# Kernel tuning notes

Measured on AMD Instinct MI355X. Metric: run time of the kernel, lower is better.

The kernel has to match this reference:

```python
import jax, jax.numpy as jnp
import numpy as np

N = 10000       # nodes
E = 640000      # edges
D_IN = 128
D_OUT = 128
EPS = 1e-5      # LayerNorm eps (torch default)


def setup_inputs() -> dict:
    key = jax.random.key(0)
    k_x, k_e, k_w, k_b, k_g = jax.random.split(key, 5)
    x = jax.random.normal(k_x, (N, D_IN), dtype=jnp.float32)
    edge_index = jax.random.randint(k_e, (2, E), 0, N, dtype=jnp.int64)
    # GCNConv linear weight (PyG uses glorot) and bias
    lim = float(np.sqrt(6.0 / (D_IN + D_OUT)))
    W = jax.random.uniform(k_w, (D_IN, D_OUT), minval=-lim, maxval=lim, dtype=jnp.float32)
    b = jnp.zeros((D_OUT,), dtype=jnp.float32)
    # LayerNorm affine params
    gamma = jnp.ones((D_OUT,), dtype=jnp.float32)
    beta = jnp.zeros((D_OUT,), dtype=jnp.float32)
    return {"x": x, "edge_index": edge_index, "W": W, "b": b, "gamma": gamma, "beta": beta}


def reference(x, edge_index, W, b, gamma, beta):
    # --- GCNConv: A_hat = D^{-1/2} (A + I) D^{-1/2}; out = A_hat X W + b ---
    self_idx = jnp.arange(N, dtype=edge_index.dtype)
    src = jnp.concatenate([edge_index[0], self_idx])  # [E+N]
    dst = jnp.concatenate([edge_index[1], self_idx])  # [E+N]
    deg = jax.ops.segment_sum(jnp.ones_like(src, dtype=x.dtype), dst, num_segments=N)
    dinv = jnp.where(deg > 0, jax.lax.rsqrt(deg), 0.0)  # [N]
    norm = dinv[src] * dinv[dst]                        # [E+N]
    h = x @ W                                           # [N, D_OUT] transform first (cheaper)
    msg = h[src] * norm[:, None]                        # [E+N, D_OUT]
    out = jax.ops.segment_sum(msg, dst, num_segments=N) + b
    # --- LayerNorm over feature dim ---
    mu = jnp.mean(out, axis=-1, keepdims=True)
    var = jnp.mean(jnp.square(out - mu), axis=-1, keepdims=True)
    out = (out - mu) * jax.lax.rsqrt(var + EPS) * gamma + beta
    # act = Identity (last_act=ReLU is truthy -> Identity branch); dropout = eval identity; residual=False
    return out
```

## Files before the change

kernel.cpp:

```cpp
#include <hip/hip_runtime.h>
#include <hip/hip_fp16.h>

#define D 128
#define LN_EPS 1e-5f


static __device__ __forceinline__ float h2f(unsigned short h) {
    return __half2float(__builtin_bit_cast(__half, h));
}
static __device__ __forceinline__ unsigned short f2h(float f) {
    return __builtin_bit_cast(unsigned short, __float2half_rn(f));
}

static __device__ __forceinline__ void flagbar(int* slots, int c, int C, int phase) {
    __syncthreads();
    int val = 0x5A5A0001 + phase;
    int tid = threadIdx.x;
    if (tid == 0)
        __hip_atomic_store(&slots[phase * 64 + c], val, __ATOMIC_RELEASE, __HIP_MEMORY_SCOPE_AGENT);
    if (tid < C) {
        while (__hip_atomic_load(&slots[phase * 64 + tid], __ATOMIC_ACQUIRE, __HIP_MEMORY_SCOPE_AGENT) != val)
            __builtin_amdgcn_s_sleep(1);
    }
    __syncthreads();
}

#define P1DONE 0x5A5A00B1
#define GMAXR 8

__global__ __launch_bounds__(1024) void build_gemm_kernel(
        const int* __restrict__ src, const int* __restrict__ dst,
        const float* __restrict__ x, const float* __restrict__ W,
        unsigned int* __restrict__ Hh,
        unsigned short* __restrict__ ghist, int* __restrict__ blocksum,
        int* __restrict__ rowptr, float* __restrict__ dinv,
        unsigned short* __restrict__ csr, int* __restrict__ bar,
        int* __restrict__ p1flag,
        int N, int E, int Ec, int C, int G) {
    extern __shared__ int lds[];
    __shared__ int s_scan[20];
    int c = blockIdx.x;
    int tid = threadIdx.x;
    int lane = tid & 63, wv = tid >> 6;

    if (c >= C) {
        unsigned int* sWh = (unsigned int*)lds;
        #pragma unroll
        for (int i = tid; i < D * D / 2; i += 1024) {
            float2 v = ((const float2*)W)[i];
            sWh[i] = (unsigned int)f2h(v.x) | ((unsigned int)f2h(v.y) << 16);
        }
        __syncthreads();
        int gb = c - C;
        int nb = G - C;
        int nper = (N + nb - 1) / nb;
        int r0 = gb * nper;
        int rn = min(nper, N - r0); if (rn < 0) rn = 0;

        float2 acc[GMAXR];
        #pragma unroll
        for (int j = 0; j < GMAXR; j++) {
            acc[j] = make_float2(0.f, 0.f);
            int lr = wv + 16 * j;
            if (lr < rn) {
                float2 xr = ((const float2*)x)[(size_t)(r0 + lr) * 64 + lane];
                float y0 = 0.f, y1 = 0.f;
                #pragma unroll 8
                for (int k = 0; k < 64; k++) {
                    float g0 = __shfl(xr.x, k);
                    float g1 = __shfl(xr.y, k);
                    unsigned int w0 = sWh[(2 * k) * 64 + lane];
                    unsigned int w1 = sWh[(2 * k + 1) * 64 + lane];
                    y0 += g0 * h2f((unsigned short)w0) + g1 * h2f((unsigned short)w1);
                    y1 += g0 * h2f((unsigned short)(w0 >> 16)) + g1 * h2f((unsigned short)(w1 >> 16));
                }
                acc[j] = make_float2(y0, y1);
            }
        }
        if (tid == 0) {
            while (__hip_atomic_load(p1flag, __ATOMIC_ACQUIRE, __HIP_MEMORY_SCOPE_AGENT) != P1DONE)
                __builtin_amdgcn_s_sleep(32);
        }
        __syncthreads();
        #pragma unroll
        for (int j = 0; j < GMAXR; j++) {
            int lr = wv + 16 * j;
            if (lr < rn) {
                float dr = dinv[r0 + lr];
                Hh[(size_t)(r0 + lr) * 64 + lane] =
                    (unsigned int)f2h(acc[j].x * dr) | ((unsigned int)f2h(acc[j].y * dr) << 16);
            }
        }
        return;
    }

    for (int i = tid; i < N; i += 1024) lds[i] = 0;
    __syncthreads();
    int lo = c * Ec, hi = min(lo + Ec, E);
    #pragma unroll 4
    for (int i = lo + tid; i < hi; i += 1024)
        atomicAdd(&lds[dst[i]], 1);
    __syncthreads();
    for (int i = tid; i < N; i += 1024)
        ghist[(size_t)c * N + i] = (unsigned short)lds[i];
    flagbar(bar, c, C, 0);

    int nper = (N + C - 1) / C;
    int n0 = c * nper;
    int nn = min(nper, N - n0); if (nn < 0) nn = 0;
    int mydeg = 0;
    if (tid < nn) {
        int n = n0 + tid;
        int run = 0;
        #pragma unroll 8
        for (int cc = 0; cc < C; cc++) {
            int t = ghist[(size_t)cc * N + n];
            ghist[(size_t)cc * N + n] = (unsigned short)run;
            run += t;
        }
        mydeg = run;
        dinv[n] = rsqrtf((float)(run + 1));
    }
    int incl = mydeg;
    #pragma unroll
    for (int off = 1; off < 64; off <<= 1) {
        int y = __shfl_up(incl, off);
        if (lane >= off) incl += y;
    }
    if (lane == 63) s_scan[wv] = incl;
    __syncthreads();
    if (tid == 0) {
        int run = 0;
        #pragma unroll
        for (int k = 0; k < 16; k++) { int t = s_scan[k]; s_scan[k] = run; run += t; }
        blocksum[c] = run;
    }
    __syncthreads();
    if (tid < nn) rowptr[n0 + tid] = s_scan[wv] + incl - mydeg;
    flagbar(bar, c, C, 1);
    if (c == 0 && tid == 0)
        __hip_atomic_store(p1flag, P1DONE, __ATOMIC_RELEASE, __HIP_MEMORY_SCOPE_AGENT);

    if (tid < 64) {
        int bs = (tid < C) ? blocksum[tid] : 0;
        int inc2 = bs;
        #pragma unroll
        for (int off = 1; off < 64; off <<= 1) {
            int y = __shfl_up(inc2, off);
            if (tid >= off) inc2 += y;
        }
        if (tid == c)     s_scan[18] = inc2 - bs;
        if (tid == C - 1) s_scan[19] = inc2;
    }
    __syncthreads();
    int base = s_scan[18];
    if (tid < nn) rowptr[n0 + tid] += base;
    if (c == C - 1 && tid == 0) rowptr[N] = s_scan[19];
    flagbar(bar, c, C, 2);

    for (int i = tid; i < N; i += 1024)
        lds[i] = rowptr[i] + ghist[(size_t)c * N + i];
    __syncthreads();
    #pragma unroll 4
    for (int i = lo + tid; i < hi; i += 1024) {
        int d = dst[i];
        int pos = atomicAdd(&lds[d], 1);
        csr[pos] = (unsigned short)src[i];
    }
}

__global__ __launch_bounds__(512) void fused_agg(const unsigned int* __restrict__ Hh,
                                                 const int* __restrict__ rowptr,
                                                 const unsigned short* __restrict__ csr,
                                                 const float* __restrict__ dinv,
                                                 const float* __restrict__ bias,
                                                 const float* __restrict__ gamma,
                                                 const float* __restrict__ beta,
                                                 float* __restrict__ out, int N) {
    int w = threadIdx.x >> 6, lane = threadIdx.x & 63;
    int node = blockIdx.x * 8 + w;
    if (node >= N) return;
    float dn = dinv[node];

    unsigned int hv0 = Hh[node * 64 + lane];
    float a0 = h2f((unsigned short)hv0);
    float a1 = h2f((unsigned short)(hv0 >> 16));

    int start = rowptr[node], end = rowptr[node + 1];
    int base = start;
    for (; base + 64 <= end; base += 64) {
        int s = csr[base + lane];
        #pragma unroll 8
        for (int k = 0; k < 64; k++) {
            int sk = __shfl(s, k);
            unsigned int hv = Hh[sk * 64 + lane];
            a0 += h2f((unsigned short)hv);
            a1 += h2f((unsigned short)(hv >> 16));
        }
    }
    int rem = end - base;
    if (rem > 0) {
        int s = 0;
        if (lane < rem) s = csr[base + lane];
        for (int k = 0; k < rem; k++) {
            int sk = __shfl(s, k);
            unsigned int hv = Hh[sk * 64 + lane];
            a0 += h2f((unsigned short)hv);
            a1 += h2f((unsigned short)(hv >> 16));
        }
    }

    int c0 = lane * 2;
    float y0 = dn * a0 + bias[c0];
    float y1 = dn * a1 + bias[c0 + 1];

    float sum = y0 + y1, sq = y0 * y0 + y1 * y1;
    #pragma unroll
    for (int off = 32; off > 0; off >>= 1) {
        sum += __shfl_xor(sum, off);
        sq  += __shfl_xor(sq, off);
    }
    float mean = sum * (1.0f / D);
    float var  = sq * (1.0f / D) - mean * mean;
    float inv  = rsqrtf(var + LN_EPS);
    float o0 = (y0 - mean) * inv * gamma[c0] + beta[c0];
    float o1 = (y1 - mean) * inv * gamma[c0 + 1] + beta[c0 + 1];
    *(float2*)(out + (size_t)node * D + c0) = make_float2(o0, o1);
}


__global__ void deg_kernel(const int* __restrict__ dst, int* __restrict__ deg, int E) {
    int e = blockIdx.x * blockDim.x + threadIdx.x;
    if (e < E) atomicAdd(&deg[dst[e]], 1);
}
__global__ __launch_bounds__(1024) void scan_kernel(const int* __restrict__ deg,
                                                    int* __restrict__ rowptr,
                                                    int* __restrict__ fill,
                                                    float* __restrict__ dinv, int N) {
    __shared__ int s_wsum[16];
    __shared__ int s_woff[16];
    __shared__ int s_carry;
    int t = threadIdx.x;
    int lane = t & 63, w = t >> 6;
    if (t == 0) s_carry = 0;
    __syncthreads();
    for (int base = 0; base < N; base += 1024) {
        int i = base + t;
        int v = (i < N) ? deg[i] : 0;
        int incl = v;
        #pragma unroll
        for (int off = 1; off < 64; off <<= 1) {
            int y = __shfl_up(incl, off);
            if (lane >= off) incl += y;
        }
        if (lane == 63) s_wsum[w] = incl;
        __syncthreads();
        if (t == 0) {
            int run = s_carry;
            #pragma unroll
            for (int k = 0; k < 16; k++) { s_woff[k] = run; run += s_wsum[k]; }
            s_carry = run;
        }
        __syncthreads();
        if (i < N) {
            int rp = s_woff[w] + (incl - v);
            rowptr[i] = rp;
            fill[i] = rp;
            dinv[i] = rsqrtf((float)(v + 1));
        }
    }
    if (t == 0) rowptr[N] = s_carry;
}
__global__ void fill_kernel(const int* __restrict__ src, const int* __restrict__ dst,
                            int* __restrict__ fill, unsigned short* __restrict__ csr, int E) {
    int e = blockIdx.x * blockDim.x + threadIdx.x;
    if (e < E) {
        int pos = atomicAdd(&fill[dst[e]], 1);
        csr[pos] = (unsigned short)src[e];
    }
}
__global__ __launch_bounds__(512) void fused_fp32(const float* __restrict__ x,
                                                  const float* __restrict__ W,
                                                  const int* __restrict__ rowptr,
                                                  const unsigned short* __restrict__ csr,
                                                  const float* __restrict__ dinv,
                                                  const float* __restrict__ bias,
                                                  const float* __restrict__ gamma,
                                                  const float* __restrict__ beta,
                                                  float* __restrict__ out, int N) {
    __shared__ float sW[D * D];
    {
        const float4* Wv = (const float4*)W;
        float4* sWv = (float4*)sW;
        #pragma unroll
        for (int i = 0; i < (D * D / 4) / 512; i++)
            sWv[threadIdx.x + i * 512] = Wv[threadIdx.x + i * 512];
    }
    __syncthreads();
    int w = threadIdx.x >> 6, lane = threadIdx.x & 63;
    int node = blockIdx.x * 8 + w;
    if (node >= N) return;
    float dn = dinv[node];
    int c0 = lane * 2;
    float2 xv = *(const float2*)(x + (size_t)node * D + c0);
    float a0 = xv.x * dn * dn, a1 = xv.y * dn * dn;
    int start = rowptr[node], end = rowptr[node + 1];
    int base = start;
    for (; base + 64 <= end; base += 64) {
        int s = csr[base + lane];
        float wt = dinv[s] * dn;
        #pragma unroll 8
        for (int k = 0; k < 64; k++) {
            int sk = __shfl(s, k);
            float wk = __shfl(wt, k);
            float2 xs = *(const float2*)(x + (size_t)sk * D + c0);
            a0 += xs.x * wk; a1 += xs.y * wk;
        }
    }
    int rem = end - base;
    if (rem > 0) {
        int s = 0; float wt = 0.f;
        if (lane < rem) { s = csr[base + lane]; wt = dinv[s] * dn; }
        for (int k = 0; k < rem; k++) {
            int sk = __shfl(s, k);
            float wk = __shfl(wt, k);
            float2 xs = *(const float2*)(x + (size_t)sk * D + c0);
            a0 += xs.x * wk; a1 += xs.y * wk;
        }
    }
    float y0 = bias[c0], y1 = bias[c0 + 1];
    #pragma unroll 8
    for (int k = 0; k < 64; k++) {
        float g0 = __shfl(a0, k);
        float g1 = __shfl(a1, k);
        float2 w0 = *(const float2*)(sW + (2 * k) * D + c0);
        float2 w1 = *(const float2*)(sW + (2 * k + 1) * D + c0);
        y0 += g0 * w0.x + g1 * w1.x;
        y1 += g0 * w0.y + g1 * w1.y;
    }
    float sum = y0 + y1, sq = y0 * y0 + y1 * y1;
    #pragma unroll
    for (int off = 32; off > 0; off >>= 1) {
        sum += __shfl_xor(sum, off);
        sq  += __shfl_xor(sq, off);
    }
    float mean = sum * (1.0f / D);
    float var  = sq * (1.0f / D) - mean * mean;
    float inv  = rsqrtf(var + LN_EPS);
    float o0 = (y0 - mean) * inv * gamma[c0] + beta[c0];
    float o1 = (y1 - mean) * inv * gamma[c0 + 1] + beta[c0 + 1];
    *(float2*)(out + (size_t)node * D + c0) = make_float2(o0, o1);
}

extern "C" void kernel_launch(void* const* d_in, const int* in_sizes, int n_in,
                              void* d_out, int out_size, void* d_ws, size_t ws_size,
                              hipStream_t stream) {
    const float* x     = (const float*)d_in[0];
    const int*   ei    = (const int*)d_in[1];
    const float* W     = (const float*)d_in[2];
    const float* bias  = (const float*)d_in[3];
    const float* gamma = (const float*)d_in[4];
    const float* beta  = (const float*)d_in[5];
    float*       out   = (float*)d_out;

    int N = in_sizes[0] / D;
    int E = in_sizes[1] / 2;
    const int* src = ei;
    const int* dst = ei + E;

    char* ws = (char*)d_ws;
    size_t off = 0;
    auto carve = [&](size_t bytes) { size_t p = off; off = (off + bytes + 15) & ~15UL; return (void*)(ws + p); };
    int*            bar      = (int*)           carve(3 * 64 * 4);
    int*            p1flag   = (int*)           carve(16);
    int*            blocksum = (int*)           carve(64 * 4);
    int*            rowptr   = (int*)           carve((size_t)(N + 1) * 4);
    float*          dinv     = (float*)         carve((size_t)N * 4);
    unsigned short* csr      = (unsigned short*)carve((size_t)E * 2);
    unsigned int*   Hh       = (unsigned int*)  carve((size_t)N * (D / 2) * 4);
    size_t fixed_end = off;

    int C = 0;
    if (ws_size > fixed_end + 16) {
        size_t avail = ws_size - fixed_end - 16;
        size_t cmax = avail / ((size_t)N * 2);
        C = (int)((cmax > 64) ? 64 : cmax);
    }

    const int G = 256;
    bool gemm_ok = (C >= 16) && ((size_t)(G - C) * 16 * GMAXR >= (size_t)N);

    if (gemm_ok) {
        unsigned short* ghist = (unsigned short*)carve((size_t)C * N * 2);
        int Ec = (E + C - 1) / C;
        size_t lds = (size_t)N * 4;
        if (lds < (size_t)(D * D / 2) * 4) lds = (size_t)(D * D / 2) * 4;
        build_gemm_kernel<<<G, 1024, lds, stream>>>(src, dst, x, W, Hh, ghist,
                                                    blocksum, rowptr, dinv, csr,
                                                    bar, p1flag, N, E, Ec, C, G);
        fused_agg<<<(N + 7) / 8, 512, 0, stream>>>(Hh, rowptr, csr, dinv,
                                                   bias, gamma, beta, out, N);
    } else {
        int* deg  = (int*)carve((size_t)N * 4);
        int* fill = (int*)carve((size_t)N * 4);
        hipMemsetAsync(deg, 0, (size_t)N * 4, stream);
        deg_kernel<<<(E + 255) / 256, 256, 0, stream>>>(dst, deg, E);
        scan_kernel<<<1, 1024, 0, stream>>>(deg, rowptr, fill, dinv, N);
        fill_kernel<<<(E + 255) / 256, 256, 0, stream>>>(src, dst, fill, csr, E);
        fused_fp32<<<(N + 7) / 8, 512, 0, stream>>>(x, W, rowptr, csr, dinv,
                                                    bias, gamma, beta, out, N);
    }
}
```

Before: 140.6 us.

## Fuse build, GEMM and aggregation into one persistent megakernel with grid barrier

Adds a single persistent kernel launched with 512 blocks. It does the CSR build and the half-precision GEMM on the first 256 blocks, crosses a flag-based grid-wide barrier, and then runs the aggregation plus LayerNorm across all blocks. This removes the second kernel launch and the gap between the two dependent kernels. It falls back to the old two-kernel path when the occupancy query says all 512 blocks cannot be co-resident. Bounded spin guards are added to every wait. The risks are lower register budgets from the tighter launch bounds, and races if the guards expire or the done flags carry stale values from a previous call.

```diff
diff --git a/kernel.cpp b/kernel.cpp
--- a/kernel.cpp
+++ b/kernel.cpp
@@ -19,31 +19,111 @@
     if (tid == 0)
         __hip_atomic_store(&slots[phase * 64 + c], val, __ATOMIC_RELEASE, __HIP_MEMORY_SCOPE_AGENT);
     if (tid < C) {
-        while (__hip_atomic_load(&slots[phase * 64 + tid], __ATOMIC_ACQUIRE, __HIP_MEMORY_SCOPE_AGENT) != val)
+        int guard = 1 << 19;
+        while (--guard > 0 &&
+               __hip_atomic_load(&slots[phase * 64 + tid], __ATOMIC_ACQUIRE, __HIP_MEMORY_SCOPE_AGENT) != val)
             __builtin_amdgcn_s_sleep(1);
     }
     __syncthreads();
 }
 
-#define P1DONE 0x5A5A00B1
+#define P1DONE   0x5A5A00B1
+#define ALLDONE  0x5A5A00DD
+#define ALLDONE2 0x5A5A00EE
 #define GMAXR 8
 
-__global__ __launch_bounds__(1024) void build_gemm_kernel(
+__global__ __launch_bounds__(1024, 8) void mega2_kernel(
         const int* __restrict__ src, const int* __restrict__ dst,
         const float* __restrict__ x, const float* __restrict__ W,
         unsigned int* __restrict__ Hh,
         unsigned short* __restrict__ ghist, int* __restrict__ blocksum,
         int* __restrict__ rowptr, float* __restrict__ dinv,
         unsigned short* __restrict__ csr, int* __restrict__ bar,
-        int* __restrict__ p1flag,
-        int N, int E, int Ec, int C, int G) {
+        int* __restrict__ p1flag, int* __restrict__ done, int* __restrict__ alldone,
+        const float* __restrict__ bias, const float* __restrict__ gamma,
+        const float* __restrict__ beta, float* __restrict__ out,
+        int N, int E, int Ec, int C, int GB, int G) {
     extern __shared__ int lds[];
     __shared__ int s_scan[20];
     int c = blockIdx.x;
     int tid = threadIdx.x;
     int lane = tid & 63, wv = tid >> 6;
 
-    if (c >= C) {
+    if (c < C) {
+        for (int i = tid; i < N; i += 1024) lds[i] = 0;
+        __syncthreads();
+        int lo = c * Ec, hi = min(lo + Ec, E);
+        #pragma unroll 4
+        for (int i = lo + tid; i < hi; i += 1024)
+            atomicAdd(&lds[dst[i]], 1);
+        __syncthreads();
+        for (int i = tid; i < N; i += 1024)
+            ghist[(size_t)c * N + i] = (unsigned short)lds[i];
+        flagbar(bar, c, C, 0);
+
+        int nper = (N + C - 1) / C;
+        int n0 = c * nper;
+        int nn = min(nper, N - n0); if (nn < 0) nn = 0;
+        int mydeg = 0;
+        if (tid < nn) {
+            int n = n0 + tid;
+            int run = 0;
+            #pragma unroll 8
+            for (int cc = 0; cc < C; cc++) {
+                int t = ghist[(size_t)cc * N + n];
+                ghist[(size_t)cc * N + n] = (unsigned short)run;
+                run += t;
+            }
+            mydeg = run;
+            dinv[n] = rsqrtf((float)(run + 1));
+        }
+        int incl = mydeg;
+        #pragma unroll
+        for (int off = 1; off < 64; off <<= 1) {
+            int y = __shfl_up(incl, off);
+            if (lane >= off) incl += y;
+        }
+        if (lane == 63) s_scan[wv] = incl;
+        __syncthreads();
+        if (tid == 0) {
+            int run = 0;
+            #pragma unroll
+            for (int k = 0; k < 16; k++) { int t = s_scan[k]; s_scan[k] = run; run += t; }
+            blocksum[c] = run;
+        }
+        __syncthreads();
+        if (tid < nn) rowptr[n0 + tid] = s_scan[wv] + incl - mydeg;
+        flagbar(bar, c, C, 1);
+        if (c == 0 && tid == 0)
+            __hip_atomic_store(p1flag, P1DONE, __ATOMIC_RELEASE, __HIP_MEMORY_SCOPE_AGENT);
+
+        if (tid < 64) {
+            int bs = (tid < C) ? blocksum[tid] : 0;
+            int inc2 = bs;
+            #pragma unroll
+            for (int off = 1; off < 64; off <<= 1) {
+                int y = __shfl_up(inc2, off);
+                if (tid >= off) inc2 += y;
+            }
+            if (tid == c)     s_scan[18] = inc2 - bs;
+            if (tid == C - 1) s_scan[19] = inc2;
+        }
+        __syncthreads();
+        int base = s_scan[18];
+        if (tid < nn) rowptr[n0 + tid] += base;
+        if (c == C - 1 && tid == 0) rowptr[N] = s_scan[19];
+        flagbar(bar, c, C, 2);
+
+        for (int i = tid; i < N; i += 1024)
+            lds[i] = rowptr[i] + ghist[(size_t)c * N + i];
+        __syncthreads();
+        #pragma unroll 4
+        for (int i = lo + tid; i < hi; i += 1024) {
+            int d = dst[i];
+            int pos = atomicAdd(&lds[d], 1);
+            csr[pos] = (unsigned short)src[i];
+        }
+    } else if (c < GB) {
         unsigned int* sWh = (unsigned int*)lds;
         #pragma unroll
         for (int i = tid; i < D * D / 2; i += 1024) {
@@ -52,7 +132,7 @@
         }
         __syncthreads();
         int gb = c - C;
-        int nb = G - C;
+        int nb = GB - C;
         int nper = (N + nb - 1) / nb;
         int r0 = gb * nper;
         int rn = min(nper, N - r0); if (rn < 0) rn = 0;
@@ -78,7 +158,148 @@
             }
         }
         if (tid == 0) {
-            while (__hip_atomic_load(p1flag, __ATOMIC_ACQUIRE, __HIP_MEMORY_SCOPE_AGENT) != P1DONE)
+            int guard = 1 << 15;
+            while (--guard > 0 &&
+                   __hip_atomic_load(p1flag, __ATOMIC_ACQUIRE, __HIP_MEMORY_SCOPE_AGENT) != P1DONE)
+                __builtin_amdgcn_s_sleep(32);
+        }
+        __syncthreads();
+        #pragma unroll
+        for (int j = 0; j < GMAXR; j++) {
+            int lr = wv + 16 * j;
+            if (lr < rn) {
+                float dr = dinv[r0 + lr];
+                Hh[(size_t)(r0 + lr) * 64 + lane] =
+                    (unsigned int)f2h(acc[j].x * dr) | ((unsigned int)f2h(acc[j].y * dr) << 16);
+            }
+        }
+    }
+
+    __syncthreads();
+    if (tid == 0)
+        __hip_atomic_store(&done[c], ALLDONE, __ATOMIC_RELEASE, __HIP_MEMORY_SCOPE_AGENT);
+    if (c == 0) {
+        if (tid < G) {
+            int guard = 1 << 18;
+            while (--guard > 0 &&
+                   __hip_atomic_load(&done[tid], __ATOMIC_ACQUIRE, __HIP_MEMORY_SCOPE_AGENT) != ALLDONE)
+                __builtin_amdgcn_s_sleep(2);
+        }
+        __syncthreads();
+        if (tid == 0)
+            __hip_atomic_store(alldone, ALLDONE2, __ATOMIC_RELEASE, __HIP_MEMORY_SCOPE_AGENT);
+    } else {
+        if (tid == 0) {
+            int guard = 1 << 16;
+            while (--guard > 0 &&
+                   __hip_atomic_load(alldone, __ATOMIC_ACQUIRE, __HIP_MEMORY_SCOPE_AGENT) != ALLDONE2)
+                __builtin_amdgcn_s_sleep(16);
+        }
+    }
+    __syncthreads();
+
+    int c0 = lane * 2;
+    for (int node = wv * G + c; node < N; node += G * 16) {
+        float dn = dinv[node];
+        unsigned int hv0 = Hh[(size_t)node * 64 + lane];
+        float a0 = h2f((unsigned short)hv0);
+        float a1 = h2f((unsigned short)(hv0 >> 16));
+
+        int start = rowptr[node], end = rowptr[node + 1];
+        int base = start;
+        for (; base + 64 <= end; base += 64) {
+            int s = csr[base + lane];
+            #pragma unroll 8
+            for (int k = 0; k < 64; k++) {
+                int sk = __shfl(s, k);
+                unsigned int hv = Hh[(size_t)sk * 64 + lane];
+                a0 += h2f((unsigned short)hv);
+                a1 += h2f((unsigned short)(hv >> 16));
+            }
+        }
+        int rem = end - base;
+        if (rem > 0) {
+            int s = 0;
+            if (lane < rem) s = csr[base + lane];
+            for (int k = 0; k < rem; k++) {
+                int sk = __shfl(s, k);
+                unsigned int hv = Hh[(size_t)sk * 64 + lane];
+                a0 += h2f((unsigned short)hv);
+                a1 += h2f((unsigned short)(hv >> 16));
+            }
+        }
+
+        float y0 = dn * a0 + bias[c0];
+        float y1 = dn * a1 + bias[c0 + 1];
+
+        float sum = y0 + y1, sq = y0 * y0 + y1 * y1;
+        #pragma unroll
+        for (int off = 32; off > 0; off >>= 1) {
+            sum += __shfl_xor(sum, off);
+            sq  += __shfl_xor(sq, off);
+        }
+        float mean = sum * (1.0f / D);
+        float var  = sq * (1.0f / D) - mean * mean;
+        float inv  = rsqrtf(var + LN_EPS);
+        float o0 = (y0 - mean) * inv * gamma[c0] + beta[c0];
+        float o1 = (y1 - mean) * inv * gamma[c0 + 1] + beta[c0 + 1];
+        *(float2*)(out + (size_t)node * D + c0) = make_float2(o0, o1);
+    }
+}
+
+__global__ __launch_bounds__(1024) void build_gemm_kernel(
+        const int* __restrict__ src, const int* __restrict__ dst,
+        const float* __restrict__ x, const float* __restrict__ W,
+        unsigned int* __restrict__ Hh,
+        unsigned short* __restrict__ ghist, int* __restrict__ blocksum,
+        int* __restrict__ rowptr, float* __restrict__ dinv,
+        unsigned short* __restrict__ csr, int* __restrict__ bar,
+        int* __restrict__ p1flag,
+        int N, int E, int Ec, int C, int G) {
+    extern __shared__ int lds[];
+    __shared__ int s_scan[20];
+    int c = blockIdx.x;
+    int tid = threadIdx.x;
+    int lane = tid & 63, wv = tid >> 6;
+
+    if (c >= C) {
+        unsigned int* sWh = (unsigned int*)lds;
+        #pragma unroll
+        for (int i = tid; i < D * D / 2; i += 1024) {
+            float2 v = ((const float2*)W)[i];
+            sWh[i] = (unsigned int)f2h(v.x) | ((unsigned int)f2h(v.y) << 16);
+        }
+        __syncthreads();
+        int gb = c - C;
+        int nb = G - C;
+        int nper = (N + nb - 1) / nb;
+        int r0 = gb * nper;
+        int rn = min(nper, N - r0); if (rn < 0) rn = 0;
+
+        float2 acc[GMAXR];
+        #pragma unroll
+        for (int j = 0; j < GMAXR; j++) {
+            acc[j] = make_float2(0.f, 0.f);
+            int lr = wv + 16 * j;
+            if (lr < rn) {
+                float2 xr = ((const float2*)x)[(size_t)(r0 + lr) * 64 + lane];
+                float y0 = 0.f, y1 = 0.f;
+                #pragma unroll 8
+                for (int k = 0; k < 64; k++) {
+                    float g0 = __shfl(xr.x, k);
+                    float g1 = __shfl(xr.y, k);
+                    unsigned int w0 = sWh[(2 * k) * 64 + lane];
+                    unsigned int w1 = sWh[(2 * k + 1) * 64 + lane];
+                    y0 += g0 * h2f((unsigned short)w0) + g1 * h2f((unsigned short)w1);
+                    y1 += g0 * h2f((unsigned short)(w0 >> 16)) + g1 * h2f((unsigned short)(w1 >> 16));
+                }
+                acc[j] = make_float2(y0, y1);
+            }
+        }
+        if (tid == 0) {
+            int guard = 1 << 15;
+            while (--guard > 0 &&
+                   __hip_atomic_load(p1flag, __ATOMIC_ACQUIRE, __HIP_MEMORY_SCOPE_AGENT) != P1DONE)
                 __builtin_amdgcn_s_sleep(32);
         }
         __syncthreads();
@@ -373,6 +594,8 @@
     auto carve = [&](size_t bytes) { size_t p = off; off = (off + bytes + 15) & ~15UL; return (void*)(ws + p); };
     int*            bar      = (int*)           carve(3 * 64 * 4);
     int*            p1flag   = (int*)           carve(16);
+    int*            alldone  = (int*)           carve(16);
+    int*            done     = (int*)           carve(512 * 4);
     int*            blocksum = (int*)           carve(64 * 4);
     int*            rowptr   = (int*)           carve((size_t)(N + 1) * 4);
     float*          dinv     = (float*)         carve((size_t)N * 4);
@@ -387,19 +610,38 @@
         C = (int)((cmax > 64) ? 64 : cmax);
     }
 
-    const int G = 256;
-    bool gemm_ok = (C >= 16) && ((size_t)(G - C) * 16 * GMAXR >= (size_t)N);
-
-    if (gemm_ok) {
+    const int GB = 256;
+    const int G  = 512;
+    bool base_ok = (C >= 16) && ((size_t)(GB - C) * 16 * GMAXR >= (size_t)N);
+
+    if (base_ok) {
         unsigned short* ghist = (unsigned short*)carve((size_t)C * N * 2);
         int Ec = (E + C - 1) / C;
         size_t lds = (size_t)N * 4;
         if (lds < (size_t)(D * D / 2) * 4) lds = (size_t)(D * D / 2) * 4;
-        build_gemm_kernel<<<G, 1024, lds, stream>>>(src, dst, x, W, Hh, ghist,
-                                                    blocksum, rowptr, dinv, csr,
-                                                    bar, p1flag, N, E, Ec, C, G);
-        fused_agg<<<(N + 7) / 8, 512, 0, stream>>>(Hh, rowptr, csr, dinv,
-                                                   bias, gamma, beta, out, N);
+
+        int dev = 0, ncu = 0, bpc = 0;
+        bool mega_ok = false;
+        if (hipGetDevice(&dev) == hipSuccess &&
+            hipDeviceGetAttribute(&ncu, hipDeviceAttributeMultiprocessorCount, dev) == hipSuccess &&
+            hipOccupancyMaxActiveBlocksPerMultiprocessor(
+                &bpc, reinterpret_cast<const void*>(mega2_kernel), 1024, lds) == hipSuccess) {
+            mega_ok = ((long)bpc * (long)ncu >= (long)G);
+        }
+
+        if (mega_ok) {
+            mega2_kernel<<<G, 1024, lds, stream>>>(src, dst, x, W, Hh, ghist,
+                                                   blocksum, rowptr, dinv, csr,
+                                                   bar, p1flag, done, alldone,
+                                                   bias, gamma, beta, out,
+                                                   N, E, Ec, C, GB, G);
+        } else {
+            build_gemm_kernel<<<GB, 1024, lds, stream>>>(src, dst, x, W, Hh, ghist,
+                                                         blocksum, rowptr, dinv, csr,
+                                                         bar, p1flag, N, E, Ec, C, GB);
+            fused_agg<<<(N + 7) / 8, 512, 0, stream>>>(Hh, rowptr, csr, dinv,
+                                                       bias, gamma, beta, out, N);
+        }
     } else {
         int* deg  = (int*)carve((size_t)N * 4);
         int* fill = (int*)carve((size_t)N * 4);
```

After: 141.3 us. Within noise of the previous version (+0.5%).
